# Optimization experiments

Hardware: AMD Instinct MI355X
Metric: run time of the kernel (lower is better)

Reference implementation:

```python
import jax, jax.numpy as jnp
import numpy as np
import math

HIDDEN = 512
NUM_HEADS = 8
HEAD_DIM = HIDDEN // NUM_HEADS
NUM_BUCKETS = 32
MAX_DISTANCE = 128


def _relative_position_bucket(rel_pos, bidirectional=True):
    # rel_pos: int32 [S, T]
    num_buckets = NUM_BUCKETS
    ret = 0
    if bidirectional:
        num_buckets //= 2
        ret = (rel_pos > 0).astype(jnp.int32) * num_buckets
        rel_pos = jnp.abs(rel_pos)
    else:
        rel_pos = -jnp.minimum(rel_pos, 0)
    max_exact = num_buckets // 2
    is_small = rel_pos < max_exact
    # guard log(0); result unused where is_small
    safe = jnp.maximum(rel_pos, 1).astype(jnp.float32)
    val_if_large = max_exact + (
        jnp.log(safe / max_exact) / math.log(MAX_DISTANCE / max_exact) * (num_buckets - max_exact)
    ).astype(jnp.int32)
    val_if_large = jnp.minimum(val_if_large, num_buckets - 1)
    return ret + jnp.where(is_small, rel_pos, val_if_large)


def setup_inputs() -> dict:
    key = jax.random.key(0)
    ks = jax.random.split(key, 6)
    B, S = 4, 2048
    std = 1.0 / math.sqrt(HIDDEN)
    inp = {
        "x": jax.random.normal(ks[0], (B, S, HIDDEN), dtype=jnp.float32),
        "Wq": jax.random.normal(ks[1], (HIDDEN, HIDDEN), dtype=jnp.float32) * std,
        "Wk": jax.random.normal(ks[2], (HIDDEN, HIDDEN), dtype=jnp.float32) * std,
        "Wv": jax.random.normal(ks[3], (HIDDEN, HIDDEN), dtype=jnp.float32) * std,
        "Wo": jax.random.normal(ks[4], (HIDDEN, HIDDEN), dtype=jnp.float32) * std,
        "bias_table": jax.random.normal(ks[5], (NUM_BUCKETS, NUM_HEADS), dtype=jnp.float32) * 0.02,
    }
    return inp


def reference(x, Wq, Wk, Wv, Wo, bias_table):
    # x: [B, S, HIDDEN]; weights: [HIDDEN, HIDDEN] (out = x @ W.T semantics folded as x @ W here
    # -- weights are random so orientation is a convention; we use x @ W).
    B, S, _ = x.shape
    T = S  # self-attention, context=None
    scale = HEAD_DIM ** -0.5

    def split_heads(t, L):
        return t.reshape(B, L, NUM_HEADS, HEAD_DIM).transpose(0, 2, 1, 3)  # [B,H,L,D]

    q = split_heads(x @ Wq, S)
    k = split_heads(x @ Wk, T)
    v = split_heads(x @ Wv, T)

    # relative position bias: [1, H, S, T]
    rel = jnp.arange(T, dtype=jnp.int32)[None, :] - jnp.arange(S, dtype=jnp.int32)[:, None]
    buckets = _relative_position_bucket(rel, bidirectional=True)  # [S, T]
    pos_bias = bias_table[buckets]  # [S, T, H]
    pos_bias = pos_bias.transpose(2, 0, 1)[None]  # [1, H, S, T]

    attn = jnp.einsum("bhsd,bhtd->bhst", q, k) * scale + pos_bias
    attn = jax.nn.softmax(attn, axis=-1)  # dropout = identity (eval)
    out = jnp.einsum("bhst,bhtd->bhsd", attn, v)
    out = out.transpose(0, 2, 1, 3).reshape(B, S, HIDDEN)
    return out @ Wo
```

## Files before the change

kernel.cpp:

```cpp
#include <hip/hip_runtime.h>
#include <hip/hip_bf16.h>
#include <math.h>

#define HIDDEN 512
#define NHEADS 8
#define HDIM 64
#define SLEN 2048
#define BATCH 4
#define NROWS (BATCH*SLEN)
#define RTAB (2*SLEN-1)
#define LOG2E 1.44269504088896340736f
#define SCALE_L2E (0.125f * LOG2E)

typedef _Float16 f16;
typedef f16 f16x8 __attribute__((ext_vector_type(8)));
typedef float f32x4 __attribute__((ext_vector_type(4)));
typedef unsigned short u16;
typedef unsigned int u32;
typedef u16 u16x4 __attribute__((ext_vector_type(4)));
typedef u16 u16x8 __attribute__((ext_vector_type(8)));
typedef u32 u32x4 __attribute__((ext_vector_type(4)));

__global__ __launch_bounds__(256) void prep(
    const float* __restrict__ x, const float* __restrict__ Wq,
    const float* __restrict__ Wk, const float* __restrict__ Wv,
    const float* __restrict__ Wo, const float* __restrict__ bias_table,
    u16* __restrict__ xh, u16* __restrict__ Wt, float* __restrict__ biasrel) {
  int bid = blockIdx.x;
  int tid = threadIdx.x;
  if (bid < 2048) {
    int i = bid * 256 + tid;
    const float4* p = (const float4*)(x + (size_t)i * 8);
    float4 a = p[0], b = p[1];
    u16x8 o;
    f16 t0 = (f16)a.x; o[0] = *(u16*)&t0;
    f16 t1 = (f16)a.y; o[1] = *(u16*)&t1;
    f16 t2 = (f16)a.z; o[2] = *(u16*)&t2;
    f16 t3 = (f16)a.w; o[3] = *(u16*)&t3;
    f16 t4 = (f16)b.x; o[4] = *(u16*)&t4;
    f16 t5 = (f16)b.y; o[5] = *(u16*)&t5;
    f16 t6 = (f16)b.z; o[6] = *(u16*)&t6;
    f16 t7 = (f16)b.w; o[7] = *(u16*)&t7;
    *(u16x8*)(xh + (size_t)i * 8) = o;
  } else if (bid < 2560) {
    int wb = bid - 2048;
    int wy = wb >> 7;
    const float* W = wy == 0 ? Wq : wy == 1 ? Wk : wy == 2 ? Wv : Wo;
    u16* dst = Wt + (size_t)wy * HIDDEN * HIDDEN;
    int t = (wb & 127) * 256 + tid;
    int k = t >> 6, n0 = (t & 63) << 3;
    const float4* p = (const float4*)(W + (size_t)k * HIDDEN + n0);
    float4 a = p[0], b = p[1];
    float vals[8] = {a.x, a.y, a.z, a.w, b.x, b.y, b.z, b.w};
#pragma unroll
    for (int j = 0; j < 8; ++j) {
      f16 hv = (f16)vals[j];
      dst[(size_t)(n0 + j) * HIDDEN + k] = *(u16*)&hv;
    }
  } else {
    int i = (bid - 2560) * 256 + tid;
    if (i >= NHEADS * RTAB) return;
    int h = i / RTAB;
    int idx = i - h * RTAB;
    int rel = idx - (SLEN - 1);
    int ret = rel > 0 ? 16 : 0;
    int a = rel < 0 ? -rel : rel;
    int bidx;
    if (a < 8) {
      bidx = a;
    } else {
      float val = logf((float)a * 0.125f) / logf(16.0f) * 8.0f;
      bidx = 8 + (int)val;
      if (bidx > 15) bidx = 15;
    }
    biasrel[i] = bias_table[(ret + bidx) * NHEADS + h] * LOG2E;
  }
}

__global__ __launch_bounds__(256) void gemm_mfma(
    const u16* __restrict__ A, const u16* __restrict__ Wt0,
    const u16* __restrict__ Wt1, const u16* __restrict__ Wt2,
    void* __restrict__ O, int mode) {
  __shared__ u16 sm[2 * 128 * 72];
  u16 (*As)[72] = (u16(*)[72])sm;
  u16 (*Bs)[72] = (u16(*)[72])(sm + 128 * 72);
  const u16* Wt = blockIdx.z == 0 ? Wt0 : blockIdx.z == 1 ? Wt1 : Wt2;
  const int tid = threadIdx.x;
  const int w = tid >> 6, l = tid & 63;
  const int lr = l & 15, lg = l >> 4;
  const int wr = w >> 1, wc = w & 1;
  const int m0 = blockIdx.x << 7, n0 = blockIdx.y << 7;
  const int vtmode = (mode == 1) && (blockIdx.z == 2);

  f32x4 acc[4][4] = {};

  u16x8 areg[4], breg[4];
#pragma unroll
  for (int e = 0; e < 4; ++e) {
    int c = (e << 8) + tid;
    int row = c >> 3, g = c & 7;
    areg[e] = *(const u16x8*)(A + (size_t)(m0 + row) * HIDDEN + (g << 3));
    breg[e] = *(const u16x8*)(Wt + (size_t)(n0 + row) * HIDDEN + (g << 3));
  }

  for (int k0 = 0; k0 < HIDDEN; k0 += 64) {
    __syncthreads();
#pragma unroll
    for (int e = 0; e < 4; ++e) {
      int c = (e << 8) + tid;
      int row = c >> 3, g = c & 7;
      *(u16x8*)&As[row][g << 3] = areg[e];
      *(u16x8*)&Bs[row][g << 3] = breg[e];
    }
    __syncthreads();
    if (k0 + 64 < HIDDEN) {
#pragma unroll
      for (int e = 0; e < 4; ++e) {
        int c = (e << 8) + tid;
        int row = c >> 3, g = c & 7;
        areg[e] = *(const u16x8*)(A + (size_t)(m0 + row) * HIDDEN + k0 + 64 + (g << 3));
        breg[e] = *(const u16x8*)(Wt + (size_t)(n0 + row) * HIDDEN + k0 + 64 + (g << 3));
      }
    }
#pragma unroll
    for (int kk = 0; kk < 64; kk += 32) {
      f16x8 af[4], bf[4];
#pragma unroll
      for (int mt = 0; mt < 4; ++mt)
        af[mt] = *(const f16x8*)&As[(wr << 6) + (mt << 4) + lr][kk + (lg << 3)];
#pragma unroll
      for (int nt = 0; nt < 4; ++nt)
        bf[nt] = *(const f16x8*)&Bs[(wc << 6) + (nt << 4) + lr][kk + (lg << 3)];
      if (!vtmode) {
#pragma unroll
        for (int mt = 0; mt < 4; ++mt)
#pragma unroll
          for (int nt = 0; nt < 4; ++nt)
            acc[mt][nt] = __builtin_amdgcn_mfma_f32_16x16x32_f16(
                af[mt], bf[nt], acc[mt][nt], 0, 0, 0);
      } else {
#pragma unroll
        for (int i = 0; i < 4; ++i)
#pragma unroll
          for (int j = 0; j < 4; ++j)
            acc[i][j] = __builtin_amdgcn_mfma_f32_16x16x32_f16(
                bf[i], af[j], acc[i][j], 0, 0, 0);
      }
    }
  }

  if (mode == 0) {
    float* Of = (float*)O;
#pragma unroll
    for (int mt = 0; mt < 4; ++mt)
#pragma unroll
      for (int nt = 0; nt < 4; ++nt)
#pragma unroll
        for (int r = 0; r < 4; ++r) {
          int m = m0 + (wr << 6) + (mt << 4) + (lg << 2) + r;
          int n = n0 + (wc << 6) + (nt << 4) + lr;
          Of[(size_t)m * HIDDEN + n] = acc[mt][nt][r];
        }
  } else if (!vtmode) {
    __syncthreads();
    u16* tt = sm;
    const float osc = (blockIdx.z == 0) ? SCALE_L2E : 1.0f;
#pragma unroll
    for (int mt = 0; mt < 4; ++mt)
#pragma unroll
      for (int nt = 0; nt < 4; ++nt)
#pragma unroll
        for (int r = 0; r < 4; ++r) {
          int ml = (wr << 6) + (mt << 4) + (lg << 2) + r;
          int nl = (wc << 6) + (nt << 4) + lr;
          f16 hv = (f16)(acc[mt][nt][r] * osc);
          tt[ml * 136 + nl] = *(u16*)&hv;
        }
    __syncthreads();
    u16* O16 = (u16*)O + (size_t)blockIdx.z * NROWS * HIDDEN;
    int b = m0 >> 11, s0 = m0 & (SLEN - 1);
    int hl = tid >> 7, rr = tid & 127;
    int hh = (n0 >> 6) + hl;
    u16* obase = O16 + (((size_t)b * NHEADS + hh) * SLEN + s0) * HDIM;
#pragma unroll
    for (int c = 0; c < 8; ++c) {
      int sl = (rr >> 3) + (c << 4);
      int d8 = (rr & 7) << 3;
      u16x8 v = *(const u16x8*)&tt[sl * 136 + (hl << 6) + d8];
      *(u16x8*)(obase + (size_t)sl * HDIM + d8) = v;
    }
  } else {
    __syncthreads();
    u16* tt = sm;
#pragma unroll
    for (int i = 0; i < 4; ++i)
#pragma unroll
      for (int j = 0; j < 4; ++j)
#pragma unroll
        for (int r = 0; r < 4; ++r) {
          int nl = (wc << 6) + (i << 4) + (lg << 2) + r;
          int ml = (wr << 6) + (j << 4) + lr;
          f16 hv = (f16)acc[i][j][r];
          tt[nl * 136 + ml] = *(u16*)&hv;
        }
    __syncthreads();
    u16* O16 = (u16*)O + (size_t)2 * NROWS * HIDDEN;
    int nl = tid >> 1, half = tid & 1;
    int n = n0 + nl;
    int h = n >> 6, d = n & 63;
    int b = m0 >> 11, s_base = m0 & (SLEN - 1);
    u16* orow = O16 + (((size_t)b * NHEADS + h) * HDIM + d) * SLEN + s_base;
    const u16* trow = tt + nl * 136;
#pragma unroll
    for (int c = 0; c < 8; ++c) {
      int v_off = (half << 6) + (c << 3);
      int c0 = (v_off & ~31) | (((v_off >> 3) & 3) << 2);
      u16x4 lo = *(const u16x4*)(trow + c0);
      u16x4 hi = *(const u16x4*)(trow + c0 + 16);
      u16x8 st;
#pragma unroll
      for (int j = 0; j < 4; ++j) { st[j] = lo[j]; st[j + 4] = hi[j]; }
      *(u16x8*)(orow + v_off) = st;
    }
  }
}

__global__ __launch_bounds__(512, 4) void flash_attn_mfma(
    const u16* __restrict__ qg, const u16* __restrict__ kg,
    const u16* __restrict__ vtg, const float* __restrict__ biasrel,
    u16* __restrict__ attn_out) {
  __shared__ u16 Ks[2][64][72];
  __shared__ u16 Vt[2][64][72];

  const int tid = threadIdx.x;
  const int w = tid >> 6, l = tid & 63;
  const int lr = l & 15, lg = l >> 4;

  int bid = blockIdx.x;
  int xcd = bid & 7, idx = bid >> 3;
  int bh = (xcd << 2) + (idx >> 4);
  int bx = idx & 15;
  int h = bh & 7, b = bh >> 3;
  int q0 = bx << 7;

  const u16* qp = qg + (size_t)bh * (SLEN * HDIM);
  const u16* kp = kg + (size_t)bh * (SLEN * HDIM);
  const u16* vp = vtg + (size_t)bh * (HDIM * SLEN);

  const float bias_pos = biasrel[h * RTAB + 2 * (SLEN - 1)];
  const float bias_neg = biasrel[h * RTAB];

  f16x8 aq0, aq1;
  {
    const u16* qrow = qp + (size_t)(q0 + (w << 4) + lr) * HDIM + (lg << 3);
    aq0 = *(const f16x8*)(qrow);
    aq1 = *(const f16x8*)(qrow + 32);
  }

  const float* bb = biasrel + h * RTAB + (SLEN - 1) + (lg << 2) - lr - q0 - (w << 4);

  f32x4 acc[4] = {};
  f32x4 accl = {};
  const f16x8 ones = {(f16)1.f, (f16)1.f, (f16)1.f, (f16)1.f,
                      (f16)1.f, (f16)1.f, (f16)1.f, (f16)1.f};

  u16x8 kreg, vreg;
  {
    int row = tid >> 3, c8 = (tid & 7) << 3;
    kreg = *(const u16x8*)(kp + (size_t)row * HDIM + c8);
    vreg = *(const u16x8*)(vp + (size_t)row * SLEN + c8);
    *(u16x8*)&Ks[0][row][c8] = kreg;
    *(u16x8*)&Vt[0][row][c8] = vreg;
    kreg = *(const u16x8*)(kp + (size_t)(64 + row) * HDIM + c8);
    vreg = *(const u16x8*)(vp + (size_t)row * SLEN + 64 + c8);
  }
  __syncthreads();

  int cur = 0;
  for (int t0 = 0; t0 < SLEN; t0 += 64) {
    if (t0 + 64 < SLEN) {
      int row = tid >> 3, c8 = (tid & 7) << 3;
      *(u16x8*)&Ks[cur ^ 1][row][c8] = kreg;
      *(u16x8*)&Vt[cur ^ 1][row][c8] = vreg;
      if (t0 + 128 < SLEN) {
        kreg = *(const u16x8*)(kp + (size_t)(t0 + 128 + row) * HDIM + c8);
        vreg = *(const u16x8*)(vp + (size_t)row * SLEN + t0 + 128 + c8);
      }
    }

    int dtq = t0 - q0;
    f32x4 sc[4];
    if (dtq >= 256 || dtq <= -192) {
      float c = (dtq > 0) ? bias_pos : bias_neg;
      f32x4 cv = {c, c, c, c};
#pragma unroll
      for (int ct = 0; ct < 4; ++ct) sc[ct] = cv;
    } else {
#pragma unroll
      for (int ct = 0; ct < 4; ++ct)
#pragma unroll
        for (int r = 0; r < 4; ++r)
          sc[ct][r] = bb[t0 + (ct << 4) + r];
    }

    f16x8 kf[4][2];
#pragma unroll
    for (int ct = 0; ct < 4; ++ct) {
      kf[ct][0] = *(const f16x8*)&Ks[cur][(ct << 4) + lr][lg << 3];
      kf[ct][1] = *(const f16x8*)&Ks[cur][(ct << 4) + lr][32 + (lg << 3)];
    }

    __builtin_amdgcn_s_setprio(1);
#pragma unroll
    for (int ct = 0; ct < 4; ++ct) {
      sc[ct] = __builtin_amdgcn_mfma_f32_16x16x32_f16(
          kf[ct][0], aq0, sc[ct], 0, 0, 0);
      sc[ct] = __builtin_amdgcn_mfma_f32_16x16x32_f16(
          kf[ct][1], aq1, sc[ct], 0, 0, 0);
    }
    __builtin_amdgcn_s_setprio(0);

#pragma unroll
    for (int ct = 0; ct < 4; ++ct)
#pragma unroll
      for (int r = 0; r < 4; ++r)
        sc[ct][r] = __builtin_amdgcn_exp2f(sc[ct][r]);

    f16x8 vf[2][4];
#pragma unroll
    for (int kb = 0; kb < 2; ++kb)
#pragma unroll
      for (int dt = 0; dt < 4; ++dt)
        vf[kb][dt] = *(const f16x8*)&Vt[cur][(dt << 4) + lr][(kb << 5) + (lg << 3)];

    __builtin_amdgcn_s_setprio(1);
#pragma unroll
    for (int kb = 0; kb < 2; ++kb) {
      u32 a0 = __builtin_bit_cast(u32,
          __builtin_amdgcn_cvt_pkrtz(sc[2 * kb][0], sc[2 * kb][1]));
      u32 a1 = __builtin_bit_cast(u32,
          __builtin_amdgcn_cvt_pkrtz(sc[2 * kb][2], sc[2 * kb][3]));
      u32 a2 = __builtin_bit_cast(u32,
          __builtin_amdgcn_cvt_pkrtz(sc[2 * kb + 1][0], sc[2 * kb + 1][1]));
      u32 a3 = __builtin_bit_cast(u32,
          __builtin_amdgcn_cvt_pkrtz(sc[2 * kb + 1][2], sc[2 * kb + 1][3]));
      u32x4 pk = {a0, a1, a2, a3};
      f16x8 pa = __builtin_bit_cast(f16x8, pk);
      accl = __builtin_amdgcn_mfma_f32_16x16x32_f16(pa, ones, accl, 0, 0, 0);
#pragma unroll
      for (int dt = 0; dt < 4; ++dt)
        acc[dt] = __builtin_amdgcn_mfma_f32_16x16x32_f16(
            pa, vf[kb][dt], acc[dt], 0, 0, 0);
    }
    __builtin_amdgcn_s_setprio(0);

    __syncthreads();
    cur ^= 1;
  }

  {
    float linv[4];
#pragma unroll
    for (int r = 0; r < 4; ++r) linv[r] = 1.f / accl[r];
    u16* op = attn_out +
              ((size_t)(b * SLEN) + q0 + (w << 4)) * HIDDEN + (h << 6);
#pragma unroll
    for (int r = 0; r < 4; ++r)
#pragma unroll
      for (int dt = 0; dt < 4; ++dt) {
        f16 hv = (f16)(acc[dt][r] * linv[r]);
        op[(size_t)((lg << 2) + r) * HIDDEN + (dt << 4) + lr] = *(u16*)&hv;
      }
  }
}

extern "C" void kernel_launch(void* const* d_in, const int* in_sizes, int n_in,
                              void* d_out, int out_size, void* d_ws, size_t ws_size,
                              hipStream_t stream) {
  const float* x          = (const float*)d_in[0];
  const float* Wq         = (const float*)d_in[1];
  const float* Wk         = (const float*)d_in[2];
  const float* Wv         = (const float*)d_in[3];
  const float* Wo         = (const float*)d_in[4];
  const float* bias_table = (const float*)d_in[5];
  float* out = (float*)d_out;

  u16* xh   = (u16*)d_ws;
  u16* wt   = xh + (size_t)NROWS * HIDDEN;
  u16* qkv  = wt + (size_t)4 * HIDDEN * HIDDEN;
  u16* attno_h = qkv + (size_t)3 * NROWS * HIDDEN;
  float* biasrel = (float*)(attno_h + (size_t)NROWS * HIDDEN);

  u16* qb = qkv;
  u16* kb = qkv + (size_t)NROWS * HIDDEN;
  u16* vb = qkv + (size_t)2 * NROWS * HIDDEN;

  prep<<<2688, 256, 0, stream>>>(x, Wq, Wk, Wv, Wo, bias_table, xh, wt, biasrel);

  u16* wtq = wt;
  u16* wtk = wt + (size_t)HIDDEN * HIDDEN;
  u16* wtv = wt + (size_t)2 * HIDDEN * HIDDEN;
  u16* wto = wt + (size_t)3 * HIDDEN * HIDDEN;

  gemm_mfma<<<dim3(NROWS / 128, HIDDEN / 128, 3), 256, 0, stream>>>(
      xh, wtq, wtk, wtv, qkv, 1);

  flash_attn_mfma<<<SLEN / 128 * BATCH * NHEADS, 512, 0, stream>>>(
      qb, kb, vb, biasrel, attno_h);

  gemm_mfma<<<dim3(NROWS / 128, HIDDEN / 128, 1), 256, 0, stream>>>(
      attno_h, wto, wto, wto, out, 0);
}
```

Baseline: 101.8 us.

## Software-pipeline QK and PV across tiles in flash attention loop

Restructures the attention loop into a two-stage software pipeline. Each phase computes QK for tile t while running the PV MFMAs for the previous tile's probabilities, then does exp and packing after a barrier. The aim is to overlap exp/convert VALU work with MFMA work, at the cost of two barriers per tile, extra live registers, and dropping the occupancy hint from launch bounds.

```diff
diff --git a/kernel.cpp b/kernel.cpp
--- a/kernel.cpp
+++ b/kernel.cpp
@@ -225,7 +225,82 @@
   }
 }
 
-__global__ __launch_bounds__(512, 4) void flash_attn_mfma(
+#define FLASH_PHASE(T0, B, O, PAX, PAY, DO_PV)                                  \
+  do {                                                                          \
+    const int t0_ = (T0);                                                       \
+    int dtq_ = t0_ - q0;                                                        \
+    f32x4 sc_[4];                                                               \
+    if (dtq_ >= 256 || dtq_ <= -192) {                                          \
+      float c_ = (dtq_ > 0) ? bias_pos : bias_neg;                              \
+      f32x4 cv_ = {c_, c_, c_, c_};                                             \
+      _Pragma("unroll") for (int ct = 0; ct < 4; ++ct) sc_[ct] = cv_;           \
+    } else {                                                                    \
+      _Pragma("unroll") for (int ct = 0; ct < 4; ++ct)                          \
+        _Pragma("unroll") for (int r = 0; r < 4; ++r)                           \
+          sc_[ct][r] = bb[t0_ + (ct << 4) + r];                                 \
+    }                                                                           \
+    {                                                                           \
+      f16x8 kf_[4][2];                                                          \
+      _Pragma("unroll") for (int ct = 0; ct < 4; ++ct) {                        \
+        kf_[ct][0] = *(const f16x8*)&Ks[B][(ct << 4) + lr][lg << 3];            \
+        kf_[ct][1] = *(const f16x8*)&Ks[B][(ct << 4) + lr][32 + (lg << 3)];     \
+      }                                                                         \
+      __builtin_amdgcn_s_setprio(1);                                            \
+      _Pragma("unroll") for (int ct = 0; ct < 4; ++ct) {                        \
+        sc_[ct] = __builtin_amdgcn_mfma_f32_16x16x32_f16(                       \
+            kf_[ct][0], aq0, sc_[ct], 0, 0, 0);                                 \
+        sc_[ct] = __builtin_amdgcn_mfma_f32_16x16x32_f16(                       \
+            kf_[ct][1], aq1, sc_[ct], 0, 0, 0);                                 \
+      }                                                                         \
+      __builtin_amdgcn_s_setprio(0);                                            \
+    }                                                                           \
+    if (DO_PV) {                                                                \
+      f16x8 vf_[2][4];                                                          \
+      _Pragma("unroll") for (int kb = 0; kb < 2; ++kb)                          \
+        _Pragma("unroll") for (int dt = 0; dt < 4; ++dt)                        \
+          vf_[kb][dt] =                                                         \
+              *(const f16x8*)&Vt[O][(dt << 4) + lr][(kb << 5) + (lg << 3)];     \
+      __builtin_amdgcn_s_setprio(1);                                            \
+      _Pragma("unroll") for (int kb = 0; kb < 2; ++kb) {                        \
+        accl = __builtin_amdgcn_mfma_f32_16x16x32_f16(PAY[kb], ones, accl,      \
+                                                      0, 0, 0);                 \
+        _Pragma("unroll") for (int dt = 0; dt < 4; ++dt)                        \
+          acc[dt] = __builtin_amdgcn_mfma_f32_16x16x32_f16(                     \
+              PAY[kb], vf_[kb][dt], acc[dt], 0, 0, 0);                          \
+      }                                                                         \
+      __builtin_amdgcn_s_setprio(0);                                            \
+    }                                                                           \
+    __syncthreads();                                                            \
+    if (t0_ + 64 < SLEN) {                                                      \
+      int row_ = tid >> 3, c8_ = (tid & 7) << 3;                                \
+      *(u16x8*)&Ks[O][row_][c8_] = kreg;                                        \
+      *(u16x8*)&Vt[O][row_][c8_] = vreg;                                        \
+      if (t0_ + 128 < SLEN) {                                                   \
+        kreg = *(const u16x8*)(kp + (size_t)(t0_ + 128 + row_) * HDIM + c8_);   \
+        vreg = *(const u16x8*)(vp + (size_t)row_ * SLEN + t0_ + 128 + c8_);     \
+      }                                                                         \
+    }                                                                           \
+    _Pragma("unroll") for (int ct = 0; ct < 4; ++ct)                            \
+      _Pragma("unroll") for (int r = 0; r < 4; ++r)                             \
+        sc_[ct][r] = __builtin_amdgcn_exp2f(sc_[ct][r]);                        \
+    _Pragma("unroll") for (int kb = 0; kb < 2; ++kb) {                          \
+      u32 a0_ = __builtin_bit_cast(                                             \
+          u32, __builtin_amdgcn_cvt_pkrtz(sc_[2 * kb][0], sc_[2 * kb][1]));     \
+      u32 a1_ = __builtin_bit_cast(                                             \
+          u32, __builtin_amdgcn_cvt_pkrtz(sc_[2 * kb][2], sc_[2 * kb][3]));     \
+      u32 a2_ = __builtin_bit_cast(                                             \
+          u32, __builtin_amdgcn_cvt_pkrtz(sc_[2 * kb + 1][0],                   \
+                                          sc_[2 * kb + 1][1]));                 \
+      u32 a3_ = __builtin_bit_cast(                                             \
+          u32, __builtin_amdgcn_cvt_pkrtz(sc_[2 * kb + 1][2],                   \
+                                          sc_[2 * kb + 1][3]));                 \
+      u32x4 pk_ = {a0_, a1_, a2_, a3_};                                         \
+      PAX[kb] = __builtin_bit_cast(f16x8, pk_);                                 \
+    }                                                                           \
+    __syncthreads();                                                            \
+  } while (0)
+
+__global__ __launch_bounds__(512) void flash_attn_mfma(
     const u16* __restrict__ qg, const u16* __restrict__ kg,
     const u16* __restrict__ vtg, const float* __restrict__ biasrel,
     u16* __restrict__ attn_out) {
@@ -263,6 +338,8 @@
   f32x4 accl = {};
   const f16x8 ones = {(f16)1.f, (f16)1.f, (f16)1.f, (f16)1.f,
                       (f16)1.f, (f16)1.f, (f16)1.f, (f16)1.f};
+
+  f16x8 paA[2], paB[2];
 
   u16x8 kreg, vreg;
   {
@@ -276,86 +353,31 @@
   }
   __syncthreads();
 
-  int cur = 0;
-  for (int t0 = 0; t0 < SLEN; t0 += 64) {
-    if (t0 + 64 < SLEN) {
-      int row = tid >> 3, c8 = (tid & 7) << 3;
-      *(u16x8*)&Ks[cur ^ 1][row][c8] = kreg;
-      *(u16x8*)&Vt[cur ^ 1][row][c8] = vreg;
-      if (t0 + 128 < SLEN) {
-        kreg = *(const u16x8*)(kp + (size_t)(t0 + 128 + row) * HDIM + c8);
-        vreg = *(const u16x8*)(vp + (size_t)row * SLEN + t0 + 128 + c8);
-      }
-    }
-
-    int dtq = t0 - q0;
-    f32x4 sc[4];
-    if (dtq >= 256 || dtq <= -192) {
-      float c = (dtq > 0) ? bias_pos : bias_neg;
-      f32x4 cv = {c, c, c, c};
-#pragma unroll
-      for (int ct = 0; ct < 4; ++ct) sc[ct] = cv;
-    } else {
-#pragma unroll
-      for (int ct = 0; ct < 4; ++ct)
-#pragma unroll
-        for (int r = 0; r < 4; ++r)
-          sc[ct][r] = bb[t0 + (ct << 4) + r];
-    }
-
-    f16x8 kf[4][2];
-#pragma unroll
-    for (int ct = 0; ct < 4; ++ct) {
-      kf[ct][0] = *(const f16x8*)&Ks[cur][(ct << 4) + lr][lg << 3];
-      kf[ct][1] = *(const f16x8*)&Ks[cur][(ct << 4) + lr][32 + (lg << 3)];
-    }
-
+  FLASH_PHASE(0, 0, 1, paA, paB, 0);
+  FLASH_PHASE(64, 1, 0, paB, paA, 1);
+  for (int p = 0; p < 15; ++p) {
+    int tA = 128 + (p << 7);
+    FLASH_PHASE(tA, 0, 1, paA, paB, 1);
+    FLASH_PHASE(tA + 64, 1, 0, paB, paA, 1);
+  }
+
+  {
+    f16x8 vf_[2][4];
+#pragma unroll
+    for (int kb = 0; kb < 2; ++kb)
+#pragma unroll
+      for (int dt = 0; dt < 4; ++dt)
+        vf_[kb][dt] = *(const f16x8*)&Vt[1][(dt << 4) + lr][(kb << 5) + (lg << 3)];
     __builtin_amdgcn_s_setprio(1);
 #pragma unroll
-    for (int ct = 0; ct < 4; ++ct) {
-      sc[ct] = __builtin_amdgcn_mfma_f32_16x16x32_f16(
-          kf[ct][0], aq0, sc[ct], 0, 0, 0);
-      sc[ct] = __builtin_amdgcn_mfma_f32_16x16x32_f16(
-          kf[ct][1], aq1, sc[ct], 0, 0, 0);
-    }
-    __builtin_amdgcn_s_setprio(0);
-
-#pragma unroll
-    for (int ct = 0; ct < 4; ++ct)
-#pragma unroll
-      for (int r = 0; r < 4; ++r)
-        sc[ct][r] = __builtin_amdgcn_exp2f(sc[ct][r]);
-
-    f16x8 vf[2][4];
-#pragma unroll
-    for (int kb = 0; kb < 2; ++kb)
-#pragma unroll
-      for (int dt = 0; dt < 4; ++dt)
-        vf[kb][dt] = *(const f16x8*)&Vt[cur][(dt << 4) + lr][(kb << 5) + (lg << 3)];
-
-    __builtin_amdgcn_s_setprio(1);
-#pragma unroll
     for (int kb = 0; kb < 2; ++kb) {
-      u32 a0 = __builtin_bit_cast(u32,
-          __builtin_amdgcn_cvt_pkrtz(sc[2 * kb][0], sc[2 * kb][1]));
-      u32 a1 = __builtin_bit_cast(u32,
-          __builtin_amdgcn_cvt_pkrtz(sc[2 * kb][2], sc[2 * kb][3]));
-      u32 a2 = __builtin_bit_cast(u32,
-          __builtin_amdgcn_cvt_pkrtz(sc[2 * kb + 1][0], sc[2 * kb + 1][1]));
-      u32 a3 = __builtin_bit_cast(u32,
-          __builtin_amdgcn_cvt_pkrtz(sc[2 * kb + 1][2], sc[2 * kb + 1][3]));
-      u32x4 pk = {a0, a1, a2, a3};
-      f16x8 pa = __builtin_bit_cast(f16x8, pk);
-      accl = __builtin_amdgcn_mfma_f32_16x16x32_f16(pa, ones, accl, 0, 0, 0);
+      accl = __builtin_amdgcn_mfma_f32_16x16x32_f16(paB[kb], ones, accl, 0, 0, 0);
 #pragma unroll
       for (int dt = 0; dt < 4; ++dt)
         acc[dt] = __builtin_amdgcn_mfma_f32_16x16x32_f16(
-            pa, vf[kb][dt], acc[dt], 0, 0, 0);
+            paB[kb], vf_[kb][dt], acc[dt], 0, 0, 0);
     }
     __builtin_amdgcn_s_setprio(0);
-
-    __syncthreads();
-    cur ^= 1;
   }
 
   {
```

After: 102.2 us. Within noise of the previous version (+0.3%).
